# Kernel optimization log

Measured on AMD Instinct MI355X. Metric: run time of the kernel, lower is better.

## Reference

```python
import jax, jax.numpy as jnp
import numpy as np

N, C, H, W = 10, 512, 40, 40
HW = H * W
OUT_CH = 128
EPS = 1e-12

def _l2norm(x, axis):
    # matches F.normalize: v / max(||v||_2, eps)
    n = jnp.sqrt(jnp.sum(x * x, axis=axis, keepdims=True))
    return x / jnp.maximum(n, EPS)

def _conv(x, w, b, pad):
    y = jax.lax.conv_general_dilated(
        x, w, window_strides=(1, 1), padding=[(pad, pad), (pad, pad)],
        dimension_numbers=('NCHW', 'OIHW', 'NCHW'))
    return y + b[None, :, None, None]

def setup_inputs() -> dict:
    key = jax.random.key(0)
    ks = jax.random.split(key, 6)
    feats = jax.random.normal(ks[0], (N, C, H, W), jnp.float32)
    SISMs = jax.random.uniform(ks[1], (N, 1, H, W), jnp.float32)
    # ResNetBlock(HW -> 128) params (Kaiming-uniform-ish fan-in bounds)
    s1 = float(1.0 / np.sqrt(HW * 9))
    s2 = float(1.0 / np.sqrt(OUT_CH * 9))
    ss = float(1.0 / np.sqrt(HW))
    w1 = jax.random.uniform(ks[2], (OUT_CH, HW, 3, 3), jnp.float32, -s1, s1)
    b1 = jnp.zeros((OUT_CH,), jnp.float32)
    w2 = jax.random.uniform(ks[3], (OUT_CH, OUT_CH, 3, 3), jnp.float32, -s2, s2)
    b2 = jnp.zeros((OUT_CH,), jnp.float32)
    ws = jax.random.uniform(ks[4], (OUT_CH, HW, 1, 1), jnp.float32, -ss, ss)
    bs = jnp.zeros((OUT_CH,), jnp.float32)
    return dict(feats=feats, SISMs=SISMs, w1=w1, b1=b1, w2=w2, b2=b2, ws=ws, bs=bs)

def reference(feats, SISMs, w1, b1, w2, b2, ws, bs):
    # SISMs supplied at (H,W): bilinear resize w/ align_corners=True at same size is identity
    NFs = _l2norm(feats, axis=1)                                   # (N,C,H,W)
    SIVs = _l2norm(jnp.mean(NFs * SISMs, axis=(-1, -2)), axis=1)   # (N,C)
    # CFM: 1x1 conv of NFs with SIVs as filters -> (N,N,H,W)
    cm = jnp.einsum('nchw,mc->nmhw', NFs, SIVs).reshape(N, N, HW)
    cm = _l2norm(cm, axis=2)
    corr = jnp.einsum('nmk,npk->nmp', cm, cm)                      # (N,N,N)
    wv = jax.nn.softmax(jnp.sum(corr, axis=2), axis=1)             # (N,N)
    CSA = jnp.sum(cm * wv[:, :, None], axis=1)                     # (N,HW)
    mn = jnp.min(CSA, axis=1, keepdims=True)
    mx = jnp.max(CSA, axis=1, keepdims=True)
    CSA = (CSA - mn) / (mx - mn + EPS)
    CSA_maps = CSA.reshape(N, 1, H, W)
    # self-correlation features: (N, HW, H, W)
    NFf = NFs.reshape(N, C, HW)
    SCFs = jnp.einsum('nci,ncj->nij', NFf, NFf).reshape(N, HW, H, W)
    # reorder channels by descending CSA evidence
    idx = jnp.argsort(-CSA, axis=1)                                # (N,HW)
    RSCFs = jnp.take_along_axis(SCFs, idx[:, :, None, None], axis=1)
    x = RSCFs * CSA_maps
    # ResNetBlock: relu(conv2(relu(conv1(x))) + shortcut_1x1(x))
    h = jax.nn.relu(_conv(x, w1, b1, 1))
    h = _conv(h, w2, b2, 1)
    sc = _conv(x, ws, bs, 0)
    return jax.nn.relu(h + sc)
```

## Files before the change

### kernel.cpp

```cpp
#include <hip/hip_runtime.h>
#include <hip/hip_bf16.h>
#include <math.h>

typedef short short8 __attribute__((ext_vector_type(8)));
typedef short short4v __attribute__((ext_vector_type(4)));
typedef float f32x4 __attribute__((ext_vector_type(4)));
typedef __hip_bfloat16 bf16;

#define KN 10
#define KC 512
#define KHW 1600
#define KH 40
#define KOC 128
#define KPW 42
#define KM 1280

__device__ __forceinline__ void gload16(const void* g, void* l) {
  __builtin_amdgcn_global_load_lds(
      (const __attribute__((address_space(1))) unsigned int*)g,
      (__attribute__((address_space(3))) unsigned int*)l, 16, 0, 0);
}

__device__ __forceinline__ double blockReduceSumD(double v) {
  __shared__ double tmpS[8];
  int lane = threadIdx.x & 63, wv = threadIdx.x >> 6;
  #pragma unroll
  for (int o = 32; o > 0; o >>= 1) v += __shfl_down(v, o);
  if (lane == 0) tmpS[wv] = v;
  __syncthreads();
  if (threadIdx.x == 0) {
    int nw = (blockDim.x + 63) >> 6;
    double s = 0;
    for (int i = 0; i < nw; i++) s += tmpS[i];
    tmpS[0] = s;
  }
  __syncthreads();
  double r = tmpS[0];
  __syncthreads();
  return r;
}

__device__ __forceinline__ double blockReduceMinD(double v) {
  __shared__ double tmpMn[8];
  int lane = threadIdx.x & 63, wv = threadIdx.x >> 6;
  #pragma unroll
  for (int o = 32; o > 0; o >>= 1) v = fmin(v, __shfl_down(v, o));
  if (lane == 0) tmpMn[wv] = v;
  __syncthreads();
  if (threadIdx.x == 0) {
    int nw = (blockDim.x + 63) >> 6;
    double s = tmpMn[0];
    for (int i = 1; i < nw; i++) s = fmin(s, tmpMn[i]);
    tmpMn[0] = s;
  }
  __syncthreads();
  double r = tmpMn[0];
  __syncthreads();
  return r;
}

__device__ __forceinline__ double blockReduceMaxD(double v) {
  __shared__ double tmpMx[8];
  int lane = threadIdx.x & 63, wv = threadIdx.x >> 6;
  #pragma unroll
  for (int o = 32; o > 0; o >>= 1) v = fmax(v, __shfl_down(v, o));
  if (lane == 0) tmpMx[wv] = v;
  __syncthreads();
  if (threadIdx.x == 0) {
    int nw = (blockDim.x + 63) >> 6;
    double s = tmpMx[0];
    for (int i = 1; i < nw; i++) s = fmax(s, tmpMx[i]);
    tmpMx[0] = s;
  }
  __syncthreads();
  double r = tmpMx[0];
  __syncthreads();
  return r;
}


__global__ void k_rnormp(const float* __restrict__ feats, double* __restrict__ ps) {
  int t = blockIdx.x * 256 + threadIdx.x;
  if (t >= KN * KHW) return;
  int ci = blockIdx.y;
  int n = t / KHW, k = t % KHW;
  const float* p = feats + (size_t)n * KC * KHW + (size_t)ci * 128 * KHW + k;
  double s = 0.0;
  for (int c = 0; c < 128; ++c) { double v = p[(size_t)c * KHW]; s += v * v; }
  ps[(size_t)ci * KN * KHW + t] = s;
}

__global__ void k_rnormc(const double* __restrict__ ps, double* __restrict__ rnorm) {
  int t = blockIdx.x * 256 + threadIdx.x;
  if (t >= KN * KHW) return;
  double s = ps[t] + ps[KN * KHW + t] + ps[2 * KN * KHW + t] + ps[3 * KN * KHW + t];
  double nn = sqrt(s);
  if (nn < 1e-12) nn = 1e-12;
  rnorm[t] = 1.0 / nn;
}

__global__ void k_nft(const float* __restrict__ feats, const double* __restrict__ rnorm,
                      const float* __restrict__ sism, bf16* __restrict__ NFT,
                      double* __restrict__ vpp) {
  __shared__ float T[32][33];
  int n = blockIdx.z, k0 = blockIdx.x * 32, c0 = blockIdx.y * 32;
  int tx = threadIdx.x, ty = threadIdx.y;
  const float* fb = feats + ((size_t)n * KC + c0) * KHW + k0;
  #pragma unroll
  for (int ii = 0; ii < 4; ii++) {
    int cl = ty * 4 + ii;
    T[cl][tx] = fb[(size_t)cl * KHW + tx];
  }
  __syncthreads();
  bf16* ob = NFT + ((size_t)n * KHW + k0) * KC + c0;
  #pragma unroll
  for (int ii = 0; ii < 4; ii++) {
    int kl = ty * 4 + ii;
    float r = (float)rnorm[n * KHW + k0 + kl];
    ob[(size_t)kl * KC + tx] = __float2bfloat16(T[tx][kl] * r);
  }
  double rs = rnorm[n * KHW + k0 + tx] * (double)sism[n * KHW + k0 + tx];
  #pragma unroll
  for (int ii = 0; ii < 4; ii++) {
    int cl = ty * 4 + ii;
    double v = (double)T[cl][tx] * rs;
    #pragma unroll
    for (int o = 16; o > 0; o >>= 1) v += __shfl_down(v, o, 32);
    if (tx == 0) vpp[((size_t)n * KC + c0 + cl) * 50 + k0 / 32] = v;
  }
}

__global__ void k_sivnorm2(const double* __restrict__ vpp, double* __restrict__ SIV) {
  int n = blockIdx.x, c = threadIdx.x;
  const double* p = vpp + ((size_t)n * KC + c) * 50;
  double acc = 0;
  #pragma unroll 5
  for (int j = 0; j < 50; j++) acc += p[j];
  acc /= (double)KHW;
  double s2 = blockReduceSumD(acc * acc);
  double nn = sqrt(s2);
  if (nn < 1e-12) nn = 1e-12;
  SIV[n * KC + c] = acc / nn;
}

__global__ void k_cmP(const float* __restrict__ feats, const double* __restrict__ SIV,
                      double* __restrict__ cmp) {
  __shared__ double sv[KN][64];
  int kc = blockIdx.x, ci = blockIdx.y, n = blockIdx.z;
  for (int t = threadIdx.x; t < KN * 64; t += 256) {
    int m = t / 64, c = t % 64;
    sv[m][c] = SIV[m * KC + ci * 64 + c];
  }
  __syncthreads();
  int k = kc * 256 + threadIdx.x;
  if (k >= KHW) return;
  const float* f = feats + ((size_t)n * KC + ci * 64) * KHW + k;
  double acc[KN];
  #pragma unroll
  for (int m = 0; m < KN; m++) acc[m] = 0.0;
  for (int c = 0; c < 64; ++c) {
    double fv = f[(size_t)c * KHW];
    #pragma unroll
    for (int m = 0; m < KN; m++) acc[m] += fv * sv[m][c];
  }
  const size_t str = (size_t)KN * KN * KHW;
  #pragma unroll
  for (int m = 0; m < KN; m++)
    cmp[(size_t)ci * str + ((size_t)n * KN + m) * KHW + k] = acc[m];
}

__global__ void k_cmB(const double* __restrict__ cmp, const double* __restrict__ rnorm,
                      double* __restrict__ cm) {
  size_t t = (size_t)blockIdx.x * 256 + threadIdx.x;
  if (t >= (size_t)KN * KN * KHW) return;
  int k = t % KHW;
  int n = (int)(t / ((size_t)KN * KHW));
  const size_t str = (size_t)KN * KN * KHW;
  double s = 0;
  #pragma unroll
  for (int ci = 0; ci < 8; ci++) s += cmp[ci * str + t];
  cm[t] = s * rnorm[n * KHW + k];
}

__global__ void k_cmnorm(double* __restrict__ cm) {
  double* row = cm + (size_t)blockIdx.x * KHW;
  double s = 0;
  for (int k = threadIdx.x; k < KHW; k += 256) { double v = row[k]; s += v * v; }
  s = blockReduceSumD(s);
  double nn = sqrt(s);
  if (nn < 1e-12) nn = 1e-12;
  double rn = 1.0 / nn;
  for (int k = threadIdx.x; k < KHW; k += 256) row[k] *= rn;
}

__global__ void k_st(const double* __restrict__ cm, double* __restrict__ tbuf) {
  int b = blockIdx.x;
  int n = b / KN, m = b % KN;
  const double* base = cm + (size_t)n * KN * KHW;
  double acc = 0;
  for (int k = threadIdx.x; k < KHW; k += 256) {
    double S = 0;
    #pragma unroll
    for (int mm = 0; mm < KN; mm++) S += base[(size_t)mm * KHW + k];
    acc += base[(size_t)m * KHW + k] * S;
  }
  acc = blockReduceSumD(acc);
  if (threadIdx.x == 0) tbuf[b] = acc;
}

__global__ void k_csa(const double* __restrict__ cm, const double* __restrict__ tbuf,
                      double* __restrict__ CSAd, float* __restrict__ CSAf) {
  __shared__ double w[KN];
  int n = blockIdx.x, tid = threadIdx.x;
  if (tid == 0) {
    double v[KN], mx = -1e300;
    #pragma unroll
    for (int m = 0; m < KN; m++) { v[m] = tbuf[n * KN + m]; mx = fmax(mx, v[m]); }
    double s = 0;
    #pragma unroll
    for (int m = 0; m < KN; m++) { v[m] = exp(v[m] - mx); s += v[m]; }
    #pragma unroll
    for (int m = 0; m < KN; m++) w[m] = v[m] / s;
  }
  __syncthreads();
  double v[7];
  int cnt = 0;
  double lmin = 1e300, lmax = -1e300;
  for (int k = tid; k < KHW; k += 256) {
    double a = 0;
    #pragma unroll
    for (int m = 0; m < KN; m++) a += cm[((size_t)n * KN + m) * KHW + k] * w[m];
    v[cnt++] = a;
    lmin = fmin(lmin, a);
    lmax = fmax(lmax, a);
  }
  double mn = blockReduceMinD(lmin);
  double mx = blockReduceMaxD(lmax);
  double inv = 1.0 / (mx - mn + 1e-12);
  cnt = 0;
  for (int k = tid; k < KHW; k += 256) {
    double nv = (v[cnt++] - mn) * inv;
    CSAd[(size_t)n * KHW + k] = nv;
    CSAf[(size_t)n * KHW + k] = (float)nv;
  }
}

__global__ void k_rank(const double* __restrict__ CSAd, int* __restrict__ idx) {
  __shared__ double key[KHW];
  int b = blockIdx.x;
  int n = b / 100, it = b % 100;
  const double* src = CSAd + (size_t)n * KHW;
  for (int j = threadIdx.x; j < KHW; j += 256) key[j] = src[j];
  __syncthreads();
  int wave = threadIdx.x >> 6, lane = threadIdx.x & 63;
  int i0 = it * 16 + wave * 4;
  double ki[4];
  #pragma unroll
  for (int ii = 0; ii < 4; ii++) ki[ii] = key[i0 + ii];
  int r[4] = {0, 0, 0, 0};
  #pragma unroll
  for (int q = 0; q < 25; q++) {
    int j = q * 64 + lane;
    double kj = key[j];
    #pragma unroll
    for (int ii = 0; ii < 4; ii++) {
      int i = i0 + ii;
      r[ii] += (kj > ki[ii]) || (kj == ki[ii] && j < i);
    }
  }
  #pragma unroll
  for (int ii = 0; ii < 4; ii++) {
    int v = r[ii];
    #pragma unroll
    for (int o = 32; o > 0; o >>= 1) v += __shfl_down(v, o);
    if (lane == 0) idx[n * KHW + v] = i0 + ii;
  }
}

__global__ void k_prepw1s(const float* __restrict__ w1, const float* __restrict__ wsc,
                          bf16* __restrict__ w1s) {
  int t = blockIdx.x * 256 + threadIdx.x;
  int m = t / KHW, i = t % KHW;
  int tau = m >> 7, o = m & 127;
  float v = (tau < 9) ? w1[((size_t)o * KHW + i) * 9 + tau]
                      : wsc[(size_t)o * KHW + i];
  w1s[t] = __float2bfloat16(v);
}

__global__ void k_prepw2(const float* __restrict__ w2, bf16* __restrict__ w2p) {
  int t = blockIdx.x * 256 + threadIdx.x;
  if (t >= KOC * 9 * KOC) return;
  int o = t / (9 * KOC), r = t % (9 * KOC);
  int s = r / KOC, i = r % KOC;
  w2p[t] = __float2bfloat16(w2[(size_t)o * 9 * KOC + (size_t)i * 9 + s]);
}

__global__ void k_gath2(const short* __restrict__ NFT, const int* __restrict__ idx,
                        short* __restrict__ NFcg) {
  __shared__ short T[32][33];
  int i0 = blockIdx.x * 32, c0 = blockIdx.y * 32, n = blockIdx.z;
  int tx = threadIdx.x, ty = threadIdx.y;
  #pragma unroll
  for (int ii = 0; ii < 4; ii++) {
    int row = ty * 4 + ii;
    int id = idx[n * KHW + i0 + row];
    T[row][tx] = NFT[((size_t)n * KHW + id) * KC + c0 + tx];
  }
  __syncthreads();
  #pragma unroll
  for (int ii = 0; ii < 4; ii++) {
    int cl = ty * 4 + ii;
    NFcg[((size_t)n * KC + c0 + cl) * KHW + i0 + tx] = T[tx][cl];
  }
}

__global__ void k_zprep(const bf16* __restrict__ NFT, const float* __restrict__ CSAf,
                        bf16* __restrict__ Zpad) {
  int t = blockIdx.x * 256 + threadIdx.x;
  const int per_n = KHW * (KC / 4);
  int n = t / per_n, r = t % per_n;
  int p = r / (KC / 4), cq = r % (KC / 4);
  float cs = CSAf[n * KHW + p];
  const short* src = (const short*)(NFT + ((size_t)n * KHW + p) * KC) + cq * 4;
  short4v v = *(const short4v*)src;
  short4v o;
  #pragma unroll
  for (int j = 0; j < 4; j++) {
    short s = v[j];
    bf16 hb = *reinterpret_cast<bf16*>(&s);
    bf16 res = __float2bfloat16(__bfloat162float(hb) * cs);
    o[j] = *reinterpret_cast<short*>(&res);
  }
  int y = p / KH, x = p % KH;
  short* dst = (short*)(Zpad + ((size_t)n * KPW * KPW + (size_t)(y + 1) * KPW + (x + 1)) * KC) + cq * 4;
  *(short4v*)dst = o;
}

__global__ __launch_bounds__(256) void k_gemmU(const short* __restrict__ w1s,
                                               const short* __restrict__ NFcg,
                                               bf16* __restrict__ Uc,
                                               bf16* __restrict__ Usc) {
  __shared__ __align__(16) short smem[8704];
  short* As = smem;
  short* Bs = smem + 2048;
  short* Cs = smem;
  int b = blockIdx.x;
  int workid = (b & 7) * 100 + (b >> 3);
  int pair = workid / 20;
  int th = workid % 20;
  int n = pair >> 2, c0 = (pair & 3) * 128;
  int tau = th >> 1, half = th & 1;
  int m0 = tau * 128 + half * 64;
  int tid = threadIdx.x, lane = tid & 63, wave = tid >> 6;
  int quad = lane >> 4, l15 = lane & 15;
  int wm = (wave & 1) * 32, wn = (wave >> 1) * 64;
  int ar = tid >> 2, ko = (tid & 3) * 8;
  const short* Bb = NFcg + (size_t)n * KC * KHW;
  const short* pa0 = w1s + (size_t)(m0 + ar) * KHW + ko;
  const short* pb0 = Bb + (size_t)(c0 + ar) * KHW + ko;
  const short* pb1 = Bb + (size_t)(c0 + ar + 64) * KHW + ko;
  char* dA  = (char*)As + tid * 16;
  char* dB0 = (char*)Bs + tid * 16;
  char* dB1 = (char*)Bs + 4096 + tid * 16;
  f32x4 acc[2][4] = {};
  for (int k0 = 0; k0 < KHW; k0 += 32) {
    __syncthreads();
    gload16(pa0 + k0, dA);
    gload16(pb0 + k0, dB0);
    gload16(pb1 + k0, dB1);
    __syncthreads();
    short8 a[2], bb[4];
    #pragma unroll
    for (int t = 0; t < 2; t++) a[t] = *(const short8*)&As[(wm + t * 16 + l15) * 32 + quad * 8];
    #pragma unroll
    for (int t = 0; t < 4; t++) bb[t] = *(const short8*)&Bs[(wn + t * 16 + l15) * 32 + quad * 8];
    #pragma unroll
    for (int ti = 0; ti < 2; ti++)
      #pragma unroll
      for (int tj = 0; tj < 4; tj++)
        acc[ti][tj] = __builtin_amdgcn_mfma_f32_16x16x32_bf16(a[ti], bb[tj], acc[ti][tj], 0, 0, 0);
  }
  __syncthreads();
  #pragma unroll
  for (int ti = 0; ti < 2; ti++) {
    int lr = wm + ti * 16 + quad * 4;
    #pragma unroll
    for (int tj = 0; tj < 4; tj++) {
      int lc = wn + tj * 16 + l15;
      #pragma unroll
      for (int r = 0; r < 4; r++)
        *(bf16*)&Cs[(lr + r) * 136 + lc] = __float2bfloat16(acc[ti][tj][r]);
    }
  }
  __syncthreads();
  int dyq = tau / 3, dxq = tau % 3;
  #pragma unroll
  for (int pass = 0; pass < 4; pass++) {
    int row = pass * 16 + (tid >> 4);
    int col = (tid & 15) * 8;
    if (tau < 9) {
      *(float4*)&Uc[((size_t)((n * 3 + dyq) * 128 + half * 64 + row)) * 1536 + dxq * 512 + c0 + col] =
          *(const float4*)&Cs[row * 136 + col];
    } else {
      *(float4*)&Usc[((size_t)(n * 128 + half * 64 + row)) * 512 + c0 + col] =
          *(const float4*)&Cs[row * 136 + col];
    }
  }
}

__global__ __launch_bounds__(256) void k_convf(const short* __restrict__ Uc,
                                               const short* __restrict__ Usc,
                                               const short* __restrict__ Zpad,
                                               const float* __restrict__ b1,
                                               float* __restrict__ Hpart,
                                               bf16* __restrict__ hpadT) {
  __shared__ __align__(16) short smem[24576];
  short* As = smem;
  short* Bs = smem + 16384;
  short* Cs = smem;
  int b = blockIdx.x;
  int xcd = b & 7, bi = b >> 3;
  const int qch = 62, rch = 4;
  int wgid = (xcd < rch ? xcd * (qch + 1) : rch * (qch + 1) + (xcd - rch) * qch) + bi;
  bool isconv = (wgid & 1) == 0;
  int cid = wgid >> 1;
  int n = cid / 25, pt = cid % 25;
  int p0 = pt * 64;
  int tid = threadIdx.x, lane = tid & 63, wave = tid >> 6;
  int quad = lane >> 4, l15 = lane & 15;
  int wm = (wave & 1) * 64, wn = (wave >> 1) * 32;
  int sk = ((tid & 7) ^ ((tid >> 3) & 7)) * 8;
  int rowg = tid >> 3;
  const short* Zb = Zpad + (size_t)n * KPW * KPW * KC;
  const short* pA[4];
  #pragma unroll
  for (int g = 0; g < 4; g++) {
    int row = g * 32 + rowg;
    pA[g] = isconv ? Uc + ((size_t)(n * 3 * 128) + row) * 1536 + sk
                   : Usc + ((size_t)(n * 128) + row) * 512 + sk;
  }
  const short* pB[2];
  #pragma unroll
  for (int g = 0; g < 2; g++) {
    int p = p0 + g * 32 + rowg;
    int y = p / KH, x = p % KH;
    pB[g] = Zb + ((size_t)y * KPW + x) * KC + sk;
  }
  char* lA = (char*)As + tid * 16;
  char* lB = (char*)Bs + tid * 16;
  int NS = isconv ? 72 : 8;
  int bq = (l15 >> 2) & 1;
  int qx = (quad ^ (l15 & 3)) * 8;
  int koff0 = 32 * bq + qx;
  int koff1 = 32 * (1 - bq) + qx;
  f32x4 acc[4][2] = {};
  {
    int boff = isconv ? 0 : 22016;
    gload16(pA[0], lA); gload16(pA[1], lA + 4096);
    gload16(pA[2], lA + 8192); gload16(pA[3], lA + 12288);
    gload16(pB[0] + boff, lB); gload16(pB[1] + boff, lB + 4096);
  }
  for (int s = 0; s < NS; s++) {
    int cb = s & 1, nb = cb ^ 1;
    if (s + 1 < NS) {
      int s2 = s + 1, aoff, boff;
      if (isconv) {
        int dy = s2 / 24;
        int kk = (s2 - dy * 24) * 64;
        aoff = dy * 196608 + kk;
        boff = dy * 21504 + kk;
      } else {
        aoff = s2 * 64;
        boff = 22016 + s2 * 64;
      }
      char* la = lA + nb * 16384;
      char* lb = lB + nb * 8192;
      gload16(pA[0] + aoff, la); gload16(pA[1] + aoff, la + 4096);
      gload16(pA[2] + aoff, la + 8192); gload16(pA[3] + aoff, la + 12288);
      gload16(pB[0] + boff, lb); gload16(pB[1] + boff, lb + 4096);
      asm volatile("s_waitcnt vmcnt(6)" ::: "memory");
    } else {
      asm volatile("s_waitcnt vmcnt(0)" ::: "memory");
    }
    __builtin_amdgcn_s_barrier();
    __builtin_amdgcn_sched_barrier(0);
    const short* Ab = As + cb * 8192;
    const short* Bb = Bs + cb * 4096;
    #pragma unroll
    for (int ks = 0; ks < 2; ks++) {
      int ko = (ks == 0) ? koff0 : koff1;
      short8 av[4], bv[2];
      #pragma unroll
      for (int t = 0; t < 4; t++) av[t] = *(const short8*)&Ab[(wm + t * 16 + l15) * 64 + ko];
      #pragma unroll
      for (int t = 0; t < 2; t++) bv[t] = *(const short8*)&Bb[(wn + t * 16 + l15) * 64 + ko];
      #pragma unroll
      for (int ti = 0; ti < 4; ti++)
        #pragma unroll
        for (int tj = 0; tj < 2; tj++)
          acc[ti][tj] = __builtin_amdgcn_mfma_f32_16x16x32_bf16(av[ti], bv[tj], acc[ti][tj], 0, 0, 0);
    }
    __builtin_amdgcn_s_barrier();
  }
  if (isconv) {
    #pragma unroll
    for (int ti = 0; ti < 4; ti++) {
      int o = wm + ti * 16 + quad * 4;
      f32x4 bvv = *(const f32x4*)&b1[o];
      #pragma unroll
      for (int tj = 0; tj < 2; tj++) {
        int pl = wn + tj * 16 + l15;
        #pragma unroll
        for (int rr = 0; rr < 4; rr++) {
          float v = fmaxf(acc[ti][tj][rr] + bvv[rr], 0.0f);
          *(bf16*)&Cs[pl * 136 + o + rr] = __float2bfloat16(v);
        }
      }
    }
    __builtin_amdgcn_s_barrier();
    bf16* hp = hpadT + (size_t)n * KPW * KPW * KOC;
    #pragma unroll
    for (int pass = 0; pass < 4; pass++) {
      int rowp = pass * 16 + (tid >> 4);
      int colv = (tid & 15) * 8;
      int p = p0 + rowp;
      int y = p / KH, x = p % KH;
      *(short8*)((short*)hp + ((size_t)(y + 1) * KPW + (x + 1)) * KOC + colv) =
          *(const short8*)&Cs[rowp * 136 + colv];
    }
  } else {
    float* cb2 = Hpart + ((size_t)(3 * KN + n)) * KOC * KHW;
    #pragma unroll
    for (int ti = 0; ti < 4; ti++) {
      int o = wm + ti * 16 + quad * 4;
      #pragma unroll
      for (int tj = 0; tj < 2; tj++) {
        int qq = p0 + wn + tj * 16 + l15;
        #pragma unroll
        for (int rr = 0; rr < 4; rr++)
          cb2[(size_t)(o + rr) * KHW + qq] = acc[ti][tj][rr];
      }
    }
  }
}

__global__ __launch_bounds__(256) void k_conv2(const short* __restrict__ w2p,
                                               const short* __restrict__ hpadT,
                                               float* __restrict__ Cpart) {
  __shared__ __align__(16) short As[128 * 32];
  __shared__ __align__(16) short Bs[64 * 32];
  int p0 = blockIdx.x * 64, dy = blockIdx.y, n = blockIdx.z;
  int tid = threadIdx.x, lane = tid & 63, wave = tid >> 6;
  int quad = lane >> 4, l15 = lane & 15;
  int wm = (wave & 1) * 64, wn = (wave >> 1) * 32;
  int ar = tid >> 2, ko = (tid & 3) * 8;
  const short* hb = hpadT + (size_t)n * KPW * KPW * KOC;
  int pr = p0 + ar;
  int y0 = pr / KH, x0 = pr % KH;
  char* dA0 = (char*)As + tid * 16;
  char* dA1 = (char*)As + 4096 + tid * 16;
  char* dB  = (char*)Bs + tid * 16;
  f32x4 acc[4][2] = {};
  for (int dx = 0; dx < 3; ++dx) {
    const short* a0 = w2p + (size_t)ar * 9 * KOC + (dy * 3 + dx) * KOC + ko;
    const short* a1 = w2p + (size_t)(ar + 64) * 9 * KOC + (dy * 3 + dx) * KOC + ko;
    const short* b0 = hb + ((size_t)(y0 + dy) * KPW + (x0 + dx)) * KOC + ko;
    for (int k0 = 0; k0 < KOC; k0 += 32) {
      __syncthreads();
      gload16(a0 + k0, dA0);
      gload16(a1 + k0, dA1);
      gload16(b0 + k0, dB);
      __syncthreads();
      short8 a[4], bb[2];
      #pragma unroll
      for (int t = 0; t < 4; t++) a[t] = *(const short8*)&As[(wm + t * 16 + l15) * 32 + quad * 8];
      #pragma unroll
      for (int t = 0; t < 2; t++) bb[t] = *(const short8*)&Bs[(wn + t * 16 + l15) * 32 + quad * 8];
      #pragma unroll
      for (int ti = 0; ti < 4; ti++)
        #pragma unroll
        for (int tj = 0; tj < 2; tj++)
          acc[ti][tj] = __builtin_amdgcn_mfma_f32_16x16x32_bf16(a[ti], bb[tj], acc[ti][tj], 0, 0, 0);
    }
  }
  float* cb = Cpart + ((size_t)(dy * KN + n)) * KOC * KHW;
  #pragma unroll
  for (int ti = 0; ti < 4; ti++) {
    int o = wm + ti * 16 + quad * 4;
    #pragma unroll
    for (int tj = 0; tj < 2; tj++) {
      int q = p0 + wn + tj * 16 + l15;
      #pragma unroll
      for (int r = 0; r < 4; r++)
        cb[(size_t)(o + r) * KHW + q] = acc[ti][tj][r];
    }
  }
}

__global__ void k_final2(const float* __restrict__ Cpart, const float* __restrict__ Hpart,
                         const float* __restrict__ b2, const float* __restrict__ bs,
                         float* __restrict__ out) {
  int t = blockIdx.x * 256 + threadIdx.x;
  if (t >= KN * KOC * KHW) return;
  int o = (t / KHW) % KOC;
  const size_t stride = (size_t)KN * KOC * KHW;
  float v = Cpart[t] + Cpart[stride + t] + Cpart[2 * stride + t] +
            Hpart[3 * stride + t] + b2[o] + bs[o];
  out[t] = fmaxf(v, 0.0f);
}

extern "C" void kernel_launch(void* const* d_in, const int* in_sizes, int n_in,
                              void* d_out, int out_size, void* d_ws, size_t ws_size,
                              hipStream_t stream) {
  const float* feats = (const float*)d_in[0];
  const float* sisms = (const float*)d_in[1];
  const float* w1 = (const float*)d_in[2];
  const float* b1 = (const float*)d_in[3];
  const float* w2 = (const float*)d_in[4];
  const float* b2 = (const float*)d_in[5];
  const float* wsc = (const float*)d_in[6];
  const float* bsc = (const float*)d_in[7];
  float* out = (float*)d_out;

  char* w = (char*)d_ws;
  auto carve = [&](size_t bytes) -> void* {
    void* p = (void*)w;
    w += (bytes + 255) & ~(size_t)255;
    return p;
  };
  bf16* NFT   = (bf16*)carve((size_t)KN * KHW * KC * 2);
  bf16* NFcg  = (bf16*)carve((size_t)KN * KC * KHW * 2);
  bf16* Uc    = (bf16*)carve((size_t)KN * 3 * 128 * 1536 * 2);
  bf16* Usc   = (bf16*)carve((size_t)KN * 128 * 512 * 2);
  bf16* w1s   = (bf16*)carve((size_t)KM * KHW * 2);
  bf16* Zpad  = (bf16*)carve((size_t)KN * KPW * KPW * KC * 2);
  bf16* hpadT = (bf16*)carve((size_t)KN * KPW * KPW * KOC * 2);
  float* Hpart = (float*)carve((size_t)4 * KN * KOC * KHW * 4);
  float* Cpart = (float*)carve((size_t)3 * KN * KOC * KHW * 4);
  bf16* w2p   = (bf16*)carve((size_t)KOC * 9 * KOC * 2);
  double* psbuf = (double*)carve((size_t)4 * KN * KHW * 8);
  double* rnorm = (double*)carve((size_t)KN * KHW * 8);
  double* vpp   = (double*)carve((size_t)KN * KC * 50 * 8);
  double* SIV   = (double*)carve((size_t)KN * KC * 8);
  double* cmp   = (double*)carve((size_t)8 * KN * KN * KHW * 8);
  double* cm    = (double*)carve((size_t)KN * KN * KHW * 8);
  double* tbuf  = (double*)carve((size_t)KN * KN * 8);
  double* CSAd  = (double*)carve((size_t)KN * KHW * 8);
  float* CSAf   = (float*)carve((size_t)KN * KHW * 4);
  int* idxb     = (int*)carve((size_t)KN * KHW * 4);

  hipMemsetAsync(hpadT, 0, (size_t)KN * KPW * KPW * KOC * 2, stream);
  hipMemsetAsync(Zpad, 0, (size_t)KN * KPW * KPW * KC * 2, stream);

  k_rnormp<<<dim3(63, 4), 256, 0, stream>>>(feats, psbuf);
  k_rnormc<<<63, 256, 0, stream>>>(psbuf, rnorm);
  k_nft<<<dim3(50, 16, KN), dim3(32, 8), 0, stream>>>(feats, rnorm, sisms, NFT, vpp);
  k_sivnorm2<<<KN, 512, 0, stream>>>(vpp, SIV);
  k_cmP<<<dim3(7, 8, KN), 256, 0, stream>>>(feats, SIV, cmp);
  k_cmB<<<625, 256, 0, stream>>>(cmp, rnorm, cm);
  k_cmnorm<<<KN * KN, 256, 0, stream>>>(cm);
  k_st<<<KN * KN, 256, 0, stream>>>(cm, tbuf);
  k_csa<<<KN, 256, 0, stream>>>(cm, tbuf, CSAd, CSAf);
  k_rank<<<1000, 256, 0, stream>>>(CSAd, idxb);

  k_prepw1s<<<KM * KHW / 256, 256, 0, stream>>>(w1, wsc, w1s);
  k_prepw2<<<576, 256, 0, stream>>>(w2, w2p);
  k_gath2<<<dim3(50, 16, KN), dim3(32, 8), 0, stream>>>((const short*)NFT, idxb, (short*)NFcg);
  k_zprep<<<KN * KHW * (KC / 4) / 256, 256, 0, stream>>>(NFT, CSAf, Zpad);

  k_gemmU<<<800, 256, 0, stream>>>((const short*)w1s, (const short*)NFcg, Uc, Usc);
  k_convf<<<500, 256, 0, stream>>>((const short*)Uc, (const short*)Usc,
                                   (const short*)Zpad, b1, Hpart, hpadT);
  k_conv2<<<dim3(25, 3, KN), 256, 0, stream>>>((const short*)w2p, (const short*)hpadT, Cpart);
  k_final2<<<8000, 256, 0, stream>>>(Cpart, Hpart, b2, bsc, out);
}
```

Measured before the change: 296.8 us.

## Split conv1 by kernel row across blocks and pipeline conv2 loads

Conv1 is now split so each block handles a single kernel row (dy), writing fp32 partials. This raises the grid from 500 to 1000 blocks, each with a K loop of 24 steps instead of 72. A new kernel sums the three partials, adds the bias, applies ReLU and writes the padded bf16 activation. Conv2 is rewritten to use the same double-buffered, swizzled 64-wide K pipeline as conv1, with XCD-aware block remapping. The cost is an extra launch and extra fp32 partial traffic through memory.

```diff
diff --git a/kernel.cpp b/kernel.cpp
--- a/kernel.cpp
+++ b/kernel.cpp
@@ -408,76 +408,61 @@
   }
 }
 
-__global__ __launch_bounds__(256) void k_convf(const short* __restrict__ Uc,
+__global__ __launch_bounds__(256) void k_convh(const short* __restrict__ Uc,
                                                const short* __restrict__ Usc,
                                                const short* __restrict__ Zpad,
-                                               const float* __restrict__ b1,
-                                               float* __restrict__ Hpart,
-                                               bf16* __restrict__ hpadT) {
+                                               float* __restrict__ Hpart) {
   __shared__ __align__(16) short smem[24576];
   short* As = smem;
   short* Bs = smem + 16384;
-  short* Cs = smem;
   int b = blockIdx.x;
-  int xcd = b & 7, bi = b >> 3;
-  const int qch = 62, rch = 4;
-  int wgid = (xcd < rch ? xcd * (qch + 1) : rch * (qch + 1) + (xcd - rch) * qch) + bi;
-  bool isconv = (wgid & 1) == 0;
-  int cid = wgid >> 1;
-  int n = cid / 25, pt = cid % 25;
+  int wgid = (b & 7) * 125 + (b >> 3);
+  int n = wgid / 100, rest = wgid % 100;
+  int dy = rest / 25, pt = rest % 25;
   int p0 = pt * 64;
   int tid = threadIdx.x, lane = tid & 63, wave = tid >> 6;
   int quad = lane >> 4, l15 = lane & 15;
   int wm = (wave & 1) * 64, wn = (wave >> 1) * 32;
   int sk = ((tid & 7) ^ ((tid >> 3) & 7)) * 8;
   int rowg = tid >> 3;
+  bool isconv = (dy < 3);
   const short* Zb = Zpad + (size_t)n * KPW * KPW * KC;
+  const short* Abase = isconv ? Uc + ((size_t)((n * 3 + dy) * 128)) * 1536
+                              : Usc + ((size_t)(n * 128)) * 512;
+  int astr = isconv ? 1536 : 512;
   const short* pA[4];
   #pragma unroll
-  for (int g = 0; g < 4; g++) {
-    int row = g * 32 + rowg;
-    pA[g] = isconv ? Uc + ((size_t)(n * 3 * 128) + row) * 1536 + sk
-                   : Usc + ((size_t)(n * 128) + row) * 512 + sk;
-  }
+  for (int g = 0; g < 4; g++)
+    pA[g] = Abase + (size_t)(g * 32 + rowg) * astr + sk;
   const short* pB[2];
   #pragma unroll
   for (int g = 0; g < 2; g++) {
     int p = p0 + g * 32 + rowg;
     int y = p / KH, x = p % KH;
-    pB[g] = Zb + ((size_t)y * KPW + x) * KC + sk;
+    int yy = isconv ? (y + dy) : (y + 1);
+    int xx = isconv ? x : (x + 1);
+    pB[g] = Zb + ((size_t)yy * KPW + xx) * KC + sk;
   }
   char* lA = (char*)As + tid * 16;
   char* lB = (char*)Bs + tid * 16;
-  int NS = isconv ? 72 : 8;
+  int NS = isconv ? 24 : 8;
   int bq = (l15 >> 2) & 1;
   int qx = (quad ^ (l15 & 3)) * 8;
   int koff0 = 32 * bq + qx;
   int koff1 = 32 * (1 - bq) + qx;
   f32x4 acc[4][2] = {};
-  {
-    int boff = isconv ? 0 : 22016;
-    gload16(pA[0], lA); gload16(pA[1], lA + 4096);
-    gload16(pA[2], lA + 8192); gload16(pA[3], lA + 12288);
-    gload16(pB[0] + boff, lB); gload16(pB[1] + boff, lB + 4096);
-  }
+  gload16(pA[0], lA); gload16(pA[1], lA + 4096);
+  gload16(pA[2], lA + 8192); gload16(pA[3], lA + 12288);
+  gload16(pB[0], lB); gload16(pB[1], lB + 4096);
   for (int s = 0; s < NS; s++) {
     int cb = s & 1, nb = cb ^ 1;
     if (s + 1 < NS) {
-      int s2 = s + 1, aoff, boff;
-      if (isconv) {
-        int dy = s2 / 24;
-        int kk = (s2 - dy * 24) * 64;
-        aoff = dy * 196608 + kk;
-        boff = dy * 21504 + kk;
-      } else {
-        aoff = s2 * 64;
-        boff = 22016 + s2 * 64;
-      }
+      int off = (s + 1) * 64;
       char* la = lA + nb * 16384;
       char* lb = lB + nb * 8192;
-      gload16(pA[0] + aoff, la); gload16(pA[1] + aoff, la + 4096);
-      gload16(pA[2] + aoff, la + 8192); gload16(pA[3] + aoff, la + 12288);
-      gload16(pB[0] + boff, lb); gload16(pB[1] + boff, lb + 4096);
+      gload16(pA[0] + off, la); gload16(pA[1] + off, la + 4096);
+      gload16(pA[2] + off, la + 8192); gload16(pA[3] + off, la + 12288);
+      gload16(pB[0] + off, lb); gload16(pB[1] + off, lb + 4096);
       asm volatile("s_waitcnt vmcnt(6)" ::: "memory");
     } else {
       asm volatile("s_waitcnt vmcnt(0)" ::: "memory");
@@ -502,88 +487,120 @@
     }
     __builtin_amdgcn_s_barrier();
   }
-  if (isconv) {
-    #pragma unroll
-    for (int ti = 0; ti < 4; ti++) {
-      int o = wm + ti * 16 + quad * 4;
-      f32x4 bvv = *(const f32x4*)&b1[o];
-      #pragma unroll
-      for (int tj = 0; tj < 2; tj++) {
-        int pl = wn + tj * 16 + l15;
-        #pragma unroll
-        for (int rr = 0; rr < 4; rr++) {
-          float v = fmaxf(acc[ti][tj][rr] + bvv[rr], 0.0f);
-          *(bf16*)&Cs[pl * 136 + o + rr] = __float2bfloat16(v);
-        }
-      }
-    }
-    __builtin_amdgcn_s_barrier();
-    bf16* hp = hpadT + (size_t)n * KPW * KPW * KOC;
-    #pragma unroll
-    for (int pass = 0; pass < 4; pass++) {
-      int rowp = pass * 16 + (tid >> 4);
-      int colv = (tid & 15) * 8;
-      int p = p0 + rowp;
-      int y = p / KH, x = p % KH;
-      *(short8*)((short*)hp + ((size_t)(y + 1) * KPW + (x + 1)) * KOC + colv) =
-          *(const short8*)&Cs[rowp * 136 + colv];
-    }
-  } else {
-    float* cb2 = Hpart + ((size_t)(3 * KN + n)) * KOC * KHW;
-    #pragma unroll
-    for (int ti = 0; ti < 4; ti++) {
-      int o = wm + ti * 16 + quad * 4;
-      #pragma unroll
-      for (int tj = 0; tj < 2; tj++) {
-        int qq = p0 + wn + tj * 16 + l15;
-        #pragma unroll
-        for (int rr = 0; rr < 4; rr++)
-          cb2[(size_t)(o + rr) * KHW + qq] = acc[ti][tj][rr];
-      }
-    }
+  float* cbp = Hpart + ((size_t)(dy * KN + n)) * KOC * KHW;
+  #pragma unroll
+  for (int ti = 0; ti < 4; ti++) {
+    int o = wm + ti * 16 + quad * 4;
+    #pragma unroll
+    for (int tj = 0; tj < 2; tj++) {
+      int q = p0 + wn + tj * 16 + l15;
+      #pragma unroll
+      for (int r = 0; r < 4; r++)
+        cbp[(size_t)(o + r) * KHW + q] = acc[ti][tj][r];
+    }
+  }
+}
+
+__global__ void k_hprep3(const float* __restrict__ Hpart, const float* __restrict__ b1,
+                         bf16* __restrict__ hpadT) {
+  __shared__ float T[32][132];
+  int n = blockIdx.y, p0 = blockIdx.x * 32;
+  int tx = threadIdx.x, ty = threadIdx.y;
+  const size_t str = (size_t)KN * KOC * KHW;
+  const float* hb = Hpart + (size_t)n * KOC * KHW;
+  #pragma unroll
+  for (int oc = 0; oc < 16; oc++) {
+    int o = oc * 8 + ty;
+    size_t off = (size_t)o * KHW + p0 + tx;
+    T[tx][o] = fmaxf(hb[off] + hb[str + off] + hb[2 * str + off] + b1[o], 0.0f);
+  }
+  __syncthreads();
+  bf16* hp = hpadT + (size_t)n * KPW * KPW * KOC;
+  #pragma unroll
+  for (int pc = 0; pc < 4; pc++) {
+    int pl = ty * 4 + pc;
+    int pp = p0 + pl;
+    int yy = pp / KH, xx = pp % KH;
+    bf16* row = hp + ((size_t)(yy + 1) * KPW + (xx + 1)) * KOC;
+    #pragma unroll
+    for (int u = 0; u < 4; u++) row[tx * 4 + u] = __float2bfloat16(T[pl][tx * 4 + u]);
   }
 }
 
 __global__ __launch_bounds__(256) void k_conv2(const short* __restrict__ w2p,
                                                const short* __restrict__ hpadT,
                                                float* __restrict__ Cpart) {
-  __shared__ __align__(16) short As[128 * 32];
-  __shared__ __align__(16) short Bs[64 * 32];
-  int p0 = blockIdx.x * 64, dy = blockIdx.y, n = blockIdx.z;
+  __shared__ __align__(16) short smem[24576];
+  short* As = smem;
+  short* Bs = smem + 16384;
+  int b = blockIdx.x;
+  int xcd = b & 7, bi = b >> 3;
+  int wgid = (xcd < 6 ? xcd * 94 : 6 * 94 + (xcd - 6) * 93) + bi;
+  int n = wgid / 75, rest = wgid % 75;
+  int dy = rest / 25, pt = rest % 25;
+  int p0 = pt * 64;
   int tid = threadIdx.x, lane = tid & 63, wave = tid >> 6;
   int quad = lane >> 4, l15 = lane & 15;
   int wm = (wave & 1) * 64, wn = (wave >> 1) * 32;
-  int ar = tid >> 2, ko = (tid & 3) * 8;
+  int sk = ((tid & 7) ^ ((tid >> 3) & 7)) * 8;
+  int rowg = tid >> 3;
   const short* hb = hpadT + (size_t)n * KPW * KPW * KOC;
-  int pr = p0 + ar;
-  int y0 = pr / KH, x0 = pr % KH;
-  char* dA0 = (char*)As + tid * 16;
-  char* dA1 = (char*)As + 4096 + tid * 16;
-  char* dB  = (char*)Bs + tid * 16;
+  const short* pA[4];
+  #pragma unroll
+  for (int g = 0; g < 4; g++)
+    pA[g] = w2p + (size_t)(g * 32 + rowg) * (9 * KOC) + dy * 384 + sk;
+  const short* pB[2];
+  #pragma unroll
+  for (int g = 0; g < 2; g++) {
+    int p = p0 + g * 32 + rowg;
+    int y = p / KH, x = p % KH;
+    pB[g] = hb + ((size_t)(y + dy) * KPW + x) * KOC + sk;
+  }
+  char* lA = (char*)As + tid * 16;
+  char* lB = (char*)Bs + tid * 16;
+  const int NS = 6;
+  int bq = (l15 >> 2) & 1;
+  int qx = (quad ^ (l15 & 3)) * 8;
+  int koff0 = 32 * bq + qx;
+  int koff1 = 32 * (1 - bq) + qx;
   f32x4 acc[4][2] = {};
-  for (int dx = 0; dx < 3; ++dx) {
-    const short* a0 = w2p + (size_t)ar * 9 * KOC + (dy * 3 + dx) * KOC + ko;
-    const short* a1 = w2p + (size_t)(ar + 64) * 9 * KOC + (dy * 3 + dx) * KOC + ko;
-    const short* b0 = hb + ((size_t)(y0 + dy) * KPW + (x0 + dx)) * KOC + ko;
-    for (int k0 = 0; k0 < KOC; k0 += 32) {
-      __syncthreads();
-      gload16(a0 + k0, dA0);
-      gload16(a1 + k0, dA1);
-      gload16(b0 + k0, dB);
-      __syncthreads();
-      short8 a[4], bb[2];
-      #pragma unroll
-      for (int t = 0; t < 4; t++) a[t] = *(const short8*)&As[(wm + t * 16 + l15) * 32 + quad * 8];
-      #pragma unroll
-      for (int t = 0; t < 2; t++) bb[t] = *(const short8*)&Bs[(wn + t * 16 + l15) * 32 + quad * 8];
+  gload16(pA[0], lA); gload16(pA[1], lA + 4096);
+  gload16(pA[2], lA + 8192); gload16(pA[3], lA + 12288);
+  gload16(pB[0], lB); gload16(pB[1], lB + 4096);
+  for (int s = 0; s < NS; s++) {
+    int cb = s & 1, nb = cb ^ 1;
+    if (s + 1 < NS) {
+      int off = (s + 1) * 64;
+      char* la = lA + nb * 16384;
+      char* lb = lB + nb * 8192;
+      gload16(pA[0] + off, la); gload16(pA[1] + off, la + 4096);
+      gload16(pA[2] + off, la + 8192); gload16(pA[3] + off, la + 12288);
+      gload16(pB[0] + off, lb); gload16(pB[1] + off, lb + 4096);
+      asm volatile("s_waitcnt vmcnt(6)" ::: "memory");
+    } else {
+      asm volatile("s_waitcnt vmcnt(0)" ::: "memory");
+    }
+    __builtin_amdgcn_s_barrier();
+    __builtin_amdgcn_sched_barrier(0);
+    const short* Ab = As + cb * 8192;
+    const short* Bb = Bs + cb * 4096;
+    #pragma unroll
+    for (int ks = 0; ks < 2; ks++) {
+      int ko = (ks == 0) ? koff0 : koff1;
+      short8 av[4], bv[2];
+      #pragma unroll
+      for (int t = 0; t < 4; t++) av[t] = *(const short8*)&Ab[(wm + t * 16 + l15) * 64 + ko];
+      #pragma unroll
+      for (int t = 0; t < 2; t++) bv[t] = *(const short8*)&Bb[(wn + t * 16 + l15) * 64 + ko];
       #pragma unroll
       for (int ti = 0; ti < 4; ti++)
         #pragma unroll
         for (int tj = 0; tj < 2; tj++)
-          acc[ti][tj] = __builtin_amdgcn_mfma_f32_16x16x32_bf16(a[ti], bb[tj], acc[ti][tj], 0, 0, 0);
-    }
-  }
-  float* cb = Cpart + ((size_t)(dy * KN + n)) * KOC * KHW;
+          acc[ti][tj] = __builtin_amdgcn_mfma_f32_16x16x32_bf16(av[ti], bv[tj], acc[ti][tj], 0, 0, 0);
+    }
+    __builtin_amdgcn_s_barrier();
+  }
+  float* cbp = Cpart + ((size_t)(dy * KN + n)) * KOC * KHW;
   #pragma unroll
   for (int ti = 0; ti < 4; ti++) {
     int o = wm + ti * 16 + quad * 4;
@@ -592,7 +609,7 @@
       int q = p0 + wn + tj * 16 + l15;
       #pragma unroll
       for (int r = 0; r < 4; r++)
-        cb[(size_t)(o + r) * KHW + q] = acc[ti][tj][r];
+        cbp[(size_t)(o + r) * KHW + q] = acc[ti][tj][r];
     }
   }
 }
@@ -669,8 +686,9 @@
   k_zprep<<<KN * KHW * (KC / 4) / 256, 256, 0, stream>>>(NFT, CSAf, Zpad);
 
   k_gemmU<<<800, 256, 0, stream>>>((const short*)w1s, (const short*)NFcg, Uc, Usc);
-  k_convf<<<500, 256, 0, stream>>>((const short*)Uc, (const short*)Usc,
-                                   (const short*)Zpad, b1, Hpart, hpadT);
-  k_conv2<<<dim3(25, 3, KN), 256, 0, stream>>>((const short*)w2p, (const short*)hpadT, Cpart);
+  k_convh<<<1000, 256, 0, stream>>>((const short*)Uc, (const short*)Usc,
+                                    (const short*)Zpad, Hpart);
+  k_hprep3<<<dim3(50, KN), dim3(32, 8), 0, stream>>>(Hpart, b1, hpadT);
+  k_conv2<<<750, 256, 0, stream>>>((const short*)w2p, (const short*)hpadT, Cpart);
   k_final2<<<8000, 256, 0, stream>>>(Cpart, Hpart, b2, bsc, out);
 }
```

Result: no change. 301.4 us (+1.6%).
